# Kernel tuning notes

Hardware: AMD Instinct MI355X
Metric: run time of the kernel (lower is better)

## Reference

```python
import jax, jax.numpy as jnp
import numpy as np

NODE_DIM = 256
EDGE_DIM = 64
TIME_DIM = 1024
HEADS = 8
HEAD_DIM = NODE_DIM // HEADS
MLP = 2
BS, N = 32, 48
BN = BS * N
E = BS * N * (N - 1)


def _lin(k, fin, fout):
    return jax.random.normal(k, (fin, fout), dtype=jnp.float32) / np.sqrt(fin)


def _edge_index():
    idx = np.arange(N)
    src, dst = np.meshgrid(idx, idx, indexing='ij')
    m = src != dst
    src, dst = src[m], dst[m]              # [N*(N-1)] per graph
    offs = (np.arange(BS) * N)[:, None]
    row = (offs + src[None, :]).reshape(-1)
    col = (offs + dst[None, :]).reshape(-1)
    return jnp.asarray(np.stack([row, col]), dtype=jnp.int32)


def setup_inputs() -> dict:
    key = jax.random.key(0)
    ks = jax.random.split(key, 32)
    d = {
        'pos': jax.random.normal(ks[0], (BN, 3), jnp.float32),
        'h': jax.random.normal(ks[1], (BN, NODE_DIM), jnp.float32),
        'edge_attr': jax.random.normal(ks[2], (E, EDGE_DIM), jnp.float32),
        'node_mask': jnp.ones((BN, 1), jnp.float32),
        'node_time_emb': jax.random.normal(ks[3], (BN, TIME_DIM), jnp.float32),
        'edge_time_emb': jax.random.normal(ks[4], (E, TIME_DIM), jnp.float32),
        'edge_index': _edge_index(),
        # edge_emb: Linear(edge_dim+1 -> edge_dim)
        'W_ee': _lin(ks[5], EDGE_DIM + 1, EDGE_DIM), 'b_ee': jnp.zeros((EDGE_DIM,)),
        # AdaLN time MLPs (SiLU -> Linear)
        'W_nt': _lin(ks[6], TIME_DIM, 6 * NODE_DIM), 'b_nt': jnp.zeros((6 * NODE_DIM,)),
        'W_et': _lin(ks[7], TIME_DIM, 6 * EDGE_DIM), 'b_et': jnp.zeros((6 * EDGE_DIM,)),
        # Trans_Layer sparse attention
        'Wq': _lin(ks[8], NODE_DIM, NODE_DIM), 'bq': jnp.zeros((NODE_DIM,)),
        'Wk': _lin(ks[9], NODE_DIM, NODE_DIM), 'bk': jnp.zeros((NODE_DIM,)),
        'Wv': _lin(ks[10], NODE_DIM, NODE_DIM), 'bv': jnp.zeros((NODE_DIM,)),
        'We0': _lin(ks[11], EDGE_DIM, NODE_DIM),
        'We1': _lin(ks[12], EDGE_DIM, NODE_DIM),
        'W_n2e': _lin(ks[13], NODE_DIM, EDGE_DIM), 'b_n2e': jnp.zeros((EDGE_DIM,)),
        # node FFN
        'W_ff1': _lin(ks[14], NODE_DIM, MLP * NODE_DIM), 'b_ff1': jnp.zeros((MLP * NODE_DIM,)),
        'W_ff2': _lin(ks[15], MLP * NODE_DIM, NODE_DIM), 'b_ff2': jnp.zeros((NODE_DIM,)),
        # edge FFN
        'W_ff3': _lin(ks[16], EDGE_DIM, MLP * EDGE_DIM), 'b_ff3': jnp.zeros((MLP * EDGE_DIM,)),
        'W_ff4': _lin(ks[17], MLP * EDGE_DIM, EDGE_DIM), 'b_ff4': jnp.zeros((EDGE_DIM,)),
        # CondEquiUpdate
        'coors_scale': jnp.full((1,), 0.01, jnp.float32),
        'W_ut': _lin(ks[18], TIME_DIM, 2 * NODE_DIM), 'b_ut': jnp.zeros((2 * NODE_DIM,)),
        'W_ui': _lin(ks[19], 2 * NODE_DIM + EDGE_DIM + 1, NODE_DIM), 'b_ui': jnp.zeros((NODE_DIM,)),
        'W_uc1': _lin(ks[20], NODE_DIM, NODE_DIM), 'b_uc1': jnp.zeros((NODE_DIM,)),
        'W_uc2': _lin(ks[21], NODE_DIM, 1),
    }
    return d


def _ln(x):  # LayerNorm, no affine, eps=1e-6
    m = x.mean(-1, keepdims=True)
    v = ((x - m) ** 2).mean(-1, keepdims=True)
    return (x - m) * jax.lax.rsqrt(v + 1e-6)


def _modulate(x, shift, scale):
    return x * (1 + scale) + shift


def _block(pos, h, edge_attr, node_mask, node_time_emb, edge_time_emb, edge_index,
           W_ee, b_ee, W_nt, b_nt, W_et, b_et, Wq, bq, Wk, bk, Wv, bv, We0, We1,
           W_n2e, b_n2e, W_ff1, b_ff1, W_ff2, b_ff2, W_ff3, b_ff3, W_ff4, b_ff4,
           coors_scale, W_ut, b_ut, W_ui, b_ui, W_uc1, b_uc1, W_uc2):
    row, col = edge_index[0], edge_index[1]  # row = source j, col = target i
    diff = pos[row] - pos[col]                              # [E,3]
    dist = jnp.sqrt(jnp.sum(diff * diff, -1, keepdims=True) + 1e-12)  # [E,1]
    ea = jnp.concatenate([dist, edge_attr], -1) @ W_ee + b_ee

    nt = jax.nn.silu(node_time_emb) @ W_nt + b_nt
    n_sh_msa, n_sc_msa, n_g_msa, n_sh_mlp, n_sc_mlp, n_g_mlp = jnp.split(nt, 6, axis=1)
    et = jax.nn.silu(edge_time_emb) @ W_et + b_et
    e_sh_msa, e_sc_msa, e_g_msa, e_sh_mlp, e_sc_mlp, e_g_mlp = jnp.split(et, 6, axis=1)

    hh = _modulate(_ln(h), n_sh_msa, n_sc_msa)
    ea = _modulate(_ln(ea), e_sh_msa, e_sc_msa)

    # sparse multi-head attention over edges (Trans_Layer)
    q = (hh @ Wq + bq).reshape(BN, HEADS, HEAD_DIM)
    k = (hh @ Wk + bk).reshape(BN, HEADS, HEAD_DIM)
    v = (hh @ Wv + bv).reshape(BN, HEADS, HEAD_DIM)
    e0 = (ea @ We0).reshape(E, HEADS, HEAD_DIM)
    e1 = (ea @ We1).reshape(E, HEADS, HEAD_DIM)
    alpha = jnp.sum(q[col] * k[row] * e0, -1) / np.sqrt(HEAD_DIM)  # [E,H]
    mx = jax.ops.segment_max(alpha, col, num_segments=BN)
    ex = jnp.exp(alpha - mx[col])
    den = jax.ops.segment_sum(ex, col, num_segments=BN)
    att = ex / (den[col] + 1e-16)
    msg = v[row] * e1 * att[:, :, None]
    h_node = jax.ops.segment_sum(msg, col, num_segments=BN).reshape(BN, NODE_DIM)

    h_edge = (h_node[row] + h_node[col]) @ W_n2e + b_n2e

    h_node = h + n_g_msa * h_node
    h_node = _modulate(_ln(h_node), n_sh_mlp, n_sc_mlp) * node_mask
    ff = jax.nn.silu(h_node @ W_ff1 + b_ff1) @ W_ff2 + b_ff2
    h_out = (h_node + n_g_mlp * ff) * node_mask

    h_e = edge_attr + e_g_msa * h_edge
    h_e = _modulate(_ln(h_e), e_sh_mlp, e_sc_mlp)
    ffe = jax.nn.silu(h_e @ W_ff3 + b_ff3) @ W_ff4 + b_ff4
    h_edge_out = h_e + e_g_mlp * ffe

    # CondEquiUpdate: equivariant coordinate update
    h_input = jnp.concatenate([h_out[row], h_out[col], h_edge_out, dist], -1)
    nrm = jnp.linalg.norm(diff, axis=-1, keepdims=True)
    cdiff = diff / jnp.clip(nrm, 1e-8) * coors_scale        # CoorsNorm(scale_init=0.01)
    t_shift, t_scale = jnp.split(jax.nn.silu(edge_time_emb) @ W_ut + b_ut, 2, axis=1)
    inv = _modulate(_ln(h_input @ W_ui + b_ui), t_shift, t_scale)
    inv = jnp.tanh(jax.nn.silu(inv @ W_uc1 + b_uc1) @ W_uc2)  # [E,1]
    trans = cdiff * inv
    pos_out = pos + jax.ops.segment_sum(trans, row, num_segments=BN)
    return h_out, h_edge_out, pos_out


def reference(pos, h, edge_attr, node_mask, node_time_emb, edge_time_emb, edge_index,
              W_ee, b_ee, W_nt, b_nt, W_et, b_et, Wq, bq, Wk, bk, Wv, bv, We0, We1,
              W_n2e, b_n2e, W_ff1, b_ff1, W_ff2, b_ff2, W_ff3, b_ff3, W_ff4, b_ff4,
              coors_scale, W_ut, b_ut, W_ui, b_ui, W_uc1, b_uc1, W_uc2):
    return _block(pos, h, edge_attr, node_mask, node_time_emb, edge_time_emb, edge_index,
                  W_ee, b_ee, W_nt, b_nt, W_et, b_et, Wq, bq, Wk, bk, Wv, bv, We0, We1,
                  W_n2e, b_n2e, W_ff1, b_ff1, W_ff2, b_ff2, W_ff3, b_ff3, W_ff4, b_ff4,
                  coors_scale, W_ut, b_ut, W_ui, b_ui, W_uc1, b_uc1, W_uc2)
```

## Files before the change

### kernel.cpp

```cpp
#include <hip/hip_runtime.h>

typedef unsigned short u16;
typedef __attribute__((ext_vector_type(4))) u16 u16x4;
typedef __attribute__((ext_vector_type(8))) u16 u16x8;
typedef __attribute__((ext_vector_type(8))) short s16x8;
typedef __attribute__((ext_vector_type(4))) float f32x4;

#define E_CNT 72192
#define BN_CNT 1536
#define EPG 2256

__device__ __forceinline__ float b2f(u16 u) {
    union { unsigned int i; float f; } x; x.i = ((unsigned int)u) << 16; return x.f;
}
__device__ __forceinline__ u16 f2b(float f) {
    union { float f; unsigned int i; } x; x.f = f;
    unsigned int r = x.i + 0x7fffu + ((x.i >> 16) & 1u);
    return (u16)(r >> 16);
}
__device__ __forceinline__ float siluf(float x) { return x / (1.f + expf(-x)); }

__device__ __forceinline__ void gll16(const void* g, void* l) {
    __builtin_amdgcn_global_load_lds(
        (const __attribute__((address_space(1))) void*)g,
        (__attribute__((address_space(3))) void*)l, 16, 0, 0);
}

__device__ __forceinline__ float wave_ln64(float x) {
    float s = x;
    #pragma unroll
    for (int off = 1; off < 64; off <<= 1) s += __shfl_xor(s, off);
    float mean = s * 0.015625f;
    float d = x - mean;
    float v2 = d * d;
    #pragma unroll
    for (int off = 1; off < 64; off <<= 1) v2 += __shfl_xor(v2, off);
    return d * rsqrtf(v2 * 0.015625f + 1e-6f);
}

__device__ __forceinline__ float block_ln256(float x) {
    __shared__ float tmp[4];
    int t = threadIdx.x;
    float s = x;
    #pragma unroll
    for (int off = 1; off < 64; off <<= 1) s += __shfl_xor(s, off);
    if ((t & 63) == 0) tmp[t >> 6] = s;
    __syncthreads();
    float mean = (tmp[0] + tmp[1] + tmp[2] + tmp[3]) * (1.f / 256.f);
    float d = x - mean;
    float v2 = d * d;
    #pragma unroll
    for (int off = 1; off < 64; off <<= 1) v2 += __shfl_xor(v2, off);
    __syncthreads();
    if ((t & 63) == 0) tmp[t >> 6] = v2;
    __syncthreads();
    float var = (tmp[0] + tmp[1] + tmp[2] + tmp[3]) * (1.f / 256.f);
    return d * rsqrtf(var + 1e-6f);
}

template<int ACT, int OUTBF>
__global__ __launch_bounds__(256) void k_gemm(
    const u16* __restrict__ A, const u16* __restrict__ Bt,
    const float* __restrict__ bias, void* __restrict__ C,
    int M, int N, int K)
{
    __shared__ u16 As[64][40];
    __shared__ u16 Bs[64][40];
    int bn0 = blockIdx.x * 64, bm0 = blockIdx.y * 64;
    int t = threadIdx.x;
    int lane = t & 63, wave = t >> 6;
    int wm = wave >> 1, wn = wave & 1;
    int lr = t >> 2, lc = (t & 3) * 8;
    f32x4 acc[2][2] = {};
    const u16* Ap = A + (size_t)(bm0 + lr) * K + lc;
    const u16* Bp = Bt + (size_t)(bn0 + lr) * K + lc;
    int fr = lane & 15, fk = (lane >> 4) * 8;
    for (int k0 = 0; k0 < K; k0 += 32) {
        *(u16x8*)&As[lr][lc] = *(const u16x8*)(Ap + k0);
        *(u16x8*)&Bs[lr][lc] = *(const u16x8*)(Bp + k0);
        __syncthreads();
        s16x8 a0 = *(const s16x8*)&As[wm * 32 + fr][fk];
        s16x8 a1 = *(const s16x8*)&As[wm * 32 + 16 + fr][fk];
        s16x8 b0 = *(const s16x8*)&Bs[wn * 32 + fr][fk];
        s16x8 b1 = *(const s16x8*)&Bs[wn * 32 + 16 + fr][fk];
        acc[0][0] = __builtin_amdgcn_mfma_f32_16x16x32_bf16(a0, b0, acc[0][0], 0, 0, 0);
        acc[0][1] = __builtin_amdgcn_mfma_f32_16x16x32_bf16(a0, b1, acc[0][1], 0, 0, 0);
        acc[1][0] = __builtin_amdgcn_mfma_f32_16x16x32_bf16(a1, b0, acc[1][0], 0, 0, 0);
        acc[1][1] = __builtin_amdgcn_mfma_f32_16x16x32_bf16(a1, b1, acc[1][1], 0, 0, 0);
        __syncthreads();
    }
    int cIn = lane & 15, r4 = (lane >> 4) * 4;
    #pragma unroll
    for (int i = 0; i < 2; i++)
    #pragma unroll
    for (int j = 0; j < 2; j++) {
        int col = bn0 + wn * 32 + j * 16 + cIn;
        float bv = bias ? bias[col] : 0.f;
        #pragma unroll
        for (int r = 0; r < 4; r++) {
            int rowg = bm0 + wm * 32 + i * 16 + r4 + r;
            float vv = acc[i][j][r] + bv;
            if (ACT == 1) vv = siluf(vv);
            if (OUTBF) ((u16*)C)[(size_t)rowg * N + col] = f2b(vv);
            else       ((float*)C)[(size_t)rowg * N + col] = vv;
        }
    }
}

template<int ACT, int OUTBF>
__global__ __launch_bounds__(256) void k_gemm128(
    const u16* __restrict__ A, const u16* __restrict__ Bt,
    const float* __restrict__ bias, void* __restrict__ C,
    int M, int N, int K)
{
    __shared__ u16 As[3][128 * 32];
    __shared__ u16 Bs[3][128 * 32];
    const int t = threadIdx.x;
    const int lane = t & 63, wv = t >> 6;
    const int wm = wv >> 1, wn = wv & 1;
    const int nwg = gridDim.x * gridDim.y;
    const int orig = blockIdx.y * gridDim.x + blockIdx.x;
    const int q8 = nwg >> 3, r8 = nwg & 7;
    const int xcd = orig & 7, lin = orig >> 3;
    const int wgid = (xcd < r8 ? xcd * (q8 + 1) : r8 * (q8 + 1) + (xcd - r8) * q8) + lin;
    const int bxs = wgid % gridDim.x, bys = wgid / gridDim.x;
    const int bn0 = bxs * 128, bm0 = bys * 128;
    const int srow = t >> 2;
    const int scol = ((t & 3) ^ ((t >> 3) & 3)) * 8;
    const u16* Ap = A + (size_t)(bm0 + srow) * K + scol;
    const u16* Bp = Bt + (size_t)(bn0 + srow) * K + scol;
    const size_t rstep = (size_t)64 * K;
    const int woff = wv * 16 * 32;
    const int fr = lane & 15;
    const int fkc = (((lane >> 4) ^ ((fr >> 1) & 3)) * 8);
    f32x4 acc[4][4] = {};
    const int NT = K >> 5;

    auto STAGE = [&](int b, int ko) {
        gll16(Ap + ko, &As[b][woff]);
        gll16(Ap + ko + rstep, &As[b][woff + 64 * 32]);
        gll16(Bp + ko, &Bs[b][woff]);
        gll16(Bp + ko + rstep, &Bs[b][woff + 64 * 32]);
    };
    auto COMPUTE = [&](int b) {
        const u16* aBase = &As[b][wm * 64 * 32];
        const u16* bBase = &Bs[b][wn * 64 * 32];
        s16x8 af[4], bfr[4];
        #pragma unroll
        for (int m = 0; m < 4; m++) af[m] = *(const s16x8*)&aBase[(m * 16 + fr) * 32 + fkc];
        #pragma unroll
        for (int n = 0; n < 4; n++) bfr[n] = *(const s16x8*)&bBase[(n * 16 + fr) * 32 + fkc];
        #pragma unroll
        for (int m = 0; m < 4; m++)
        #pragma unroll
        for (int n = 0; n < 4; n++)
            acc[m][n] = __builtin_amdgcn_mfma_f32_16x16x32_bf16(af[m], bfr[n], acc[m][n], 0, 0, 0);
    };

    STAGE(0, 0);
    if (NT > 1) STAGE(1, 32);
    int cur = 0;
    for (int tt = 0; tt < NT; tt++) {
        if (tt + 2 < NT) STAGE((cur + 2) % 3, (tt + 2) * 32);
        __builtin_amdgcn_sched_barrier(0);
        int ahead = NT - 1 - tt; if (ahead > 2) ahead = 2;
        if (ahead == 2)      asm volatile("s_waitcnt vmcnt(8)" ::: "memory");
        else if (ahead == 1) asm volatile("s_waitcnt vmcnt(4)" ::: "memory");
        else                 asm volatile("s_waitcnt vmcnt(0)" ::: "memory");
        __builtin_amdgcn_sched_barrier(0);
        __builtin_amdgcn_s_barrier();
        COMPUTE(cur);
        __builtin_amdgcn_s_barrier();
        __builtin_amdgcn_sched_barrier(0);
        cur = (cur + 1) % 3;
    }

    const int cIn = lane & 15, r4 = (lane >> 4) * 4;
    #pragma unroll
    for (int n = 0; n < 4; n++) {
        int col = bn0 + wn * 64 + n * 16 + cIn;
        float bv = bias ? bias[col] : 0.f;
        #pragma unroll
        for (int m = 0; m < 4; m++) {
            #pragma unroll
            for (int r = 0; r < 4; r++) {
                int rowg = bm0 + wm * 64 + m * 16 + r4 + r;
                float vv = acc[m][n][r] + bv;
                if (ACT == 1) vv = siluf(vv);
                if (OUTBF) ((u16*)C)[(size_t)rowg * N + col] = f2b(vv);
                else       ((float*)C)[(size_t)rowg * N + col] = vv;
            }
        }
    }
}

struct ConvJob { const float* W; u16* Wt; int ldw, k0, n0, K, tile_start, tiles_k; };
struct CopyJob { const float* src; float* dst; int n; };
struct BatchArgs { ConvJob cj[17]; CopyJob cp[5]; int conv_blocks; };

__global__ __launch_bounds__(256) void k_prep(BatchArgs a)
{
    __shared__ float ls[64][65];
    int b = blockIdx.x;
    int t = threadIdx.x;
    if (b < a.conv_blocks) {
        int j = 0;
        #pragma unroll 1
        while (j + 1 < 17 && a.cj[j + 1].tile_start <= b) ++j;
        const ConvJob J = a.cj[j];
        int local = b - J.tile_start;
        int tk = local % J.tiles_k, tn = local / J.tiles_k;
        int k0 = tk * 64, n0 = tn * 64;
        int cn = t & 63, rk = t >> 6;
        #pragma unroll
        for (int p = 0; p < 16; p++) {
            int kk = p * 4 + rk;
            ls[kk][cn] = J.W[(size_t)(J.k0 + k0 + kk) * J.ldw + J.n0 + n0 + cn];
        }
        __syncthreads();
        int ck = t & 63, rn = t >> 6;
        #pragma unroll
        for (int p = 0; p < 16; p++) {
            int nn = p * 4 + rn;
            J.Wt[(size_t)(n0 + nn) * J.K + k0 + ck] = f2b(ls[ck][nn]);
        }
    } else {
        int c = b - a.conv_blocks;
        const CopyJob C = a.cp[c];
        for (int i = t; i < C.n; i += 256) C.dst[i] = C.src[i];
    }
}

__global__ void k_silu_bf(const float* __restrict__ in, u16* __restrict__ out, int n4)
{
    int i = blockIdx.x * 256 + threadIdx.x;
    int stride = gridDim.x * 256;
    for (; i < n4; i += stride) {
        f32x4 v = *(const f32x4*)(in + (size_t)i * 4);
        u16x4 o;
        #pragma unroll
        for (int j = 0; j < 4; j++) o[j] = f2b(siluf(v[j]));
        *(u16x4*)(out + (size_t)i * 4) = o;
    }
}

__global__ __launch_bounds__(256) void k_edge_pre(
    const float* __restrict__ pos, const float* __restrict__ edge_attr,
    const int* __restrict__ ei, const float* __restrict__ W_ee,
    const float* __restrict__ b_ee, const float* __restrict__ coors_scale,
    const u16* __restrict__ etf,
    u16* __restrict__ ea_mod, float* __restrict__ dist, float* __restrict__ cdiff)
{
    __shared__ float Ws[65][64];
    int t = threadIdx.x;
    for (int i = t; i < 65 * 64; i += 256) Ws[i >> 6][i & 63] = W_ee[i];
    __syncthreads();
    int l = t & 63;
    float bee = b_ee[l];
    float cscale = coors_scale[0];
    for (int g = 0; g < 16; g++) {
        int e = blockIdx.x * 64 + g * 4 + (t >> 6);
        int row = ei[e], col = ei[E_CNT + e];
        float d0 = pos[row * 3 + 0] - pos[col * 3 + 0];
        float d1 = pos[row * 3 + 1] - pos[col * 3 + 1];
        float d2 = pos[row * 3 + 2] - pos[col * 3 + 2];
        float ssq = d0 * d0 + d1 * d1 + d2 * d2;
        float dst = sqrtf(ssq + 1e-12f);
        float nrm = sqrtf(ssq);
        float cs = cscale / fmaxf(nrm, 1e-8f);
        if (l == 0) {
            dist[e] = dst;
            cdiff[e * 3 + 0] = d0 * cs; cdiff[e * 3 + 1] = d1 * cs; cdiff[e * 3 + 2] = d2 * cs;
        }
        float attr = edge_attr[(size_t)e * 64 + l];
        float acc = dst * Ws[0][l];
        for (int f = 0; f < 64; f++) acc += __shfl(attr, f) * Ws[1 + f][l];
        acc += bee;
        float y = wave_ln64(acc);
        const u16* ep = etf + (size_t)e * 896;
        float m = y * (1.f + b2f(ep[64 + l])) + b2f(ep[l]);
        ea_mod[(size_t)e * 64 + l] = f2b(m);
    }
}

__global__ __launch_bounds__(256) void k_node_hh(
    const float* __restrict__ h, const float* __restrict__ nt, u16* __restrict__ hh)
{
    int n = blockIdx.x, c = threadIdx.x;
    float x = h[(size_t)n * 256 + c];
    float y = block_ln256(x);
    float m = y * (1.f + nt[(size_t)n * 1536 + 256 + c]) + nt[(size_t)n * 1536 + c];
    hh[(size_t)n * 256 + c] = f2b(m);
}

__global__ __launch_bounds__(256) void k_agg(
    const float* __restrict__ qkv, const u16* __restrict__ e01,
    float* __restrict__ hnode, u16* __restrict__ hnode_bf)
{
    int n = blockIdx.x;
    int b = n / 48, i = n % 48;
    int t = threadIdx.x;
    __shared__ float qs[8][33];
    __shared__ float att[47][8];
    __shared__ float mxs[8], dens[8];
    __shared__ int elist[47], slist[47];
    qs[t >> 5][t & 31] = qkv[(size_t)n * 768 + t];
    if (t < 47) {
        int s = t + (t >= i ? 1 : 0);
        slist[t] = s;
        elist[t] = b * EPG + s * 47 + (i < s ? i : i - 1);
    }
    __syncthreads();
    for (int idx = t; idx < 376; idx += 256) {
        int j = idx >> 3, hh = idx & 7;
        int src = b * 48 + slist[j];
        int e = elist[j];
        const float* kp = qkv + (size_t)src * 768 + 256 + hh * 32;
        const u16* ep = e01 + (size_t)e * 512 + hh * 32;
        float p = 0.f;
        #pragma unroll
        for (int d = 0; d < 32; d++) p += qs[hh][d] * kp[d] * b2f(ep[d]);
        att[j][hh] = p * 0.17677669529663687f;
    }
    __syncthreads();
    if (t < 8) {
        float m = -1e30f;
        for (int j = 0; j < 47; j++) m = fmaxf(m, att[j][t]);
        float den = 0.f;
        for (int j = 0; j < 47; j++) den += expf(att[j][t] - m);
        mxs[t] = m; dens[t] = den + 1e-16f;
    }
    __syncthreads();
    for (int idx = t; idx < 376; idx += 256) {
        int j = idx >> 3, hh = idx & 7;
        att[j][hh] = expf(att[j][hh] - mxs[hh]) / dens[hh];
    }
    __syncthreads();
    int c = t, hh = t >> 5;
    float acc = 0.f;
    for (int j = 0; j < 47; j++) {
        int src = b * 48 + slist[j];
        int e = elist[j];
        acc += att[j][hh] * qkv[(size_t)src * 768 + 512 + c] * b2f(e01[(size_t)e * 512 + 256 + c]);
    }
    hnode[(size_t)n * 256 + c] = acc;
    hnode_bf[(size_t)n * 256 + c] = f2b(acc);
}

__global__ __launch_bounds__(256) void k_node_mod(
    const float* __restrict__ h, const float* __restrict__ hnode_raw,
    const float* __restrict__ nt, const float* __restrict__ mask,
    float* __restrict__ hmod, u16* __restrict__ hmod_bf)
{
    int n = blockIdx.x, c = threadIdx.x;
    float x = h[(size_t)n * 256 + c] + nt[(size_t)n * 1536 + 512 + c] * hnode_raw[(size_t)n * 256 + c];
    float y = block_ln256(x);
    float m = (y * (1.f + nt[(size_t)n * 1536 + 1024 + c]) + nt[(size_t)n * 1536 + 768 + c]) * mask[n];
    hmod[(size_t)n * 256 + c] = m;
    hmod_bf[(size_t)n * 256 + c] = f2b(m);
}

__global__ void k_hout(const float* __restrict__ hmod, const float* __restrict__ ff2,
                       const float* __restrict__ nt, const float* __restrict__ mask,
                       float* __restrict__ out, u16* __restrict__ hout_bf)
{
    int i = blockIdx.x * 256 + threadIdx.x;
    if (i >= BN_CNT * 256) return;
    int n = i >> 8, c = i & 255;
    float v = (hmod[i] + nt[(size_t)n * 1536 + 1280 + c] * ff2[i]) * mask[n];
    out[i] = v;
    hout_bf[i] = f2b(v);
}

__global__ __launch_bounds__(256) void k_edge_mod(
    const float* __restrict__ Q1, const float* __restrict__ b_n2e,
    const float* __restrict__ edge_attr, const int* __restrict__ ei,
    const u16* __restrict__ etf, float* __restrict__ hemod, u16* __restrict__ hemod_bf)
{
    int e = blockIdx.x * 4 + (threadIdx.x >> 6);
    int l = threadIdx.x & 63;
    int row = ei[e], col = ei[E_CNT + e];
    float hedge = Q1[(size_t)row * 64 + l] + Q1[(size_t)col * 64 + l] + b_n2e[l];
    const u16* ep = etf + (size_t)e * 896;
    float x = edge_attr[(size_t)e * 64 + l] + b2f(ep[128 + l]) * hedge;
    float y = wave_ln64(x);
    float m = y * (1.f + b2f(ep[256 + l])) + b2f(ep[192 + l]);
    hemod[(size_t)e * 64 + l] = m;
    hemod_bf[(size_t)e * 64 + l] = f2b(m);
}

__global__ void k_edge_out(const float* __restrict__ hemod, const float* __restrict__ ff4,
                           const u16* __restrict__ etf,
                           float* __restrict__ out2, u16* __restrict__ heout_bf)
{
    size_t i = (size_t)blockIdx.x * 256 + threadIdx.x;
    if (i >= (size_t)E_CNT * 64) return;
    int e = (int)(i >> 6), c = (int)(i & 63);
    float v = hemod[i] + b2f(etf[(size_t)e * 896 + 320 + c]) * ff4[i];
    out2[i] = v;
    heout_bf[i] = f2b(v);
}

__global__ __launch_bounds__(256) void k_inv_pre(
    const float* __restrict__ p12,
    const u16* __restrict__ P3, const float* __restrict__ dist,
    const float* __restrict__ W_ui, const float* __restrict__ b_ui,
    const int* __restrict__ ei, const u16* __restrict__ etf, u16* __restrict__ invmod)
{
    int e = blockIdx.x, c = threadIdx.x;
    int row = ei[e], col = ei[E_CNT + e];
    float x = p12[(size_t)row * 512 + c] + p12[(size_t)col * 512 + 256 + c]
            + b2f(P3[(size_t)e * 256 + c]) + dist[e] * W_ui[576 * 256 + c] + b_ui[c];
    float y = block_ln256(x);
    const u16* ep = etf + (size_t)e * 896;
    float m = y * (1.f + b2f(ep[640 + c])) + b2f(ep[384 + c]);
    invmod[(size_t)e * 256 + c] = f2b(m);
}

__global__ __launch_bounds__(256) void k_inv(const u16* __restrict__ uc1,
                                             const float* __restrict__ W_uc2,
                                             float* __restrict__ inv)
{
    int e = blockIdx.x * 4 + (threadIdx.x >> 6);
    int l = threadIdx.x & 63;
    u16x4 v = *(const u16x4*)(uc1 + (size_t)e * 256 + l * 4);
    const float* w = W_uc2 + l * 4;
    float s = b2f(v[0]) * w[0] + b2f(v[1]) * w[1] + b2f(v[2]) * w[2] + b2f(v[3]) * w[3];
    #pragma unroll
    for (int off = 1; off < 64; off <<= 1) s += __shfl_xor(s, off);
    if (l == 0) inv[e] = tanhf(s);
}

__global__ void k_pos(const float* __restrict__ pos, const float* __restrict__ cdiff,
                      const float* __restrict__ inv, float* __restrict__ out3)
{
    int n = blockIdx.x * 256 + threadIdx.x;
    if (n >= BN_CNT) return;
    int b = n / 48, s = n % 48;
    int e0 = b * EPG + s * 47;
    float a0 = 0.f, a1 = 0.f, a2 = 0.f;
    for (int j = 0; j < 47; j++) {
        float f = inv[e0 + j];
        a0 += cdiff[(size_t)(e0 + j) * 3 + 0] * f;
        a1 += cdiff[(size_t)(e0 + j) * 3 + 1] * f;
        a2 += cdiff[(size_t)(e0 + j) * 3 + 2] * f;
    }
    out3[n * 3 + 0] = pos[n * 3 + 0] + a0;
    out3[n * 3 + 1] = pos[n * 3 + 1] + a1;
    out3[n * 3 + 2] = pos[n * 3 + 2] + a2;
}

extern "C" void kernel_launch(void* const* d_in, const int* in_sizes, int n_in,
                              void* d_out, int out_size, void* d_ws, size_t ws_size,
                              hipStream_t stream)
{
    (void)in_sizes; (void)n_in; (void)out_size; (void)ws_size;
    const float* pos       = (const float*)d_in[0];
    const float* h         = (const float*)d_in[1];
    const float* edge_attr = (const float*)d_in[2];
    const float* node_mask = (const float*)d_in[3];
    const float* nte       = (const float*)d_in[4];
    const float* ete       = (const float*)d_in[5];
    const int*   ei        = (const int*)d_in[6];
    const float* W_ee = (const float*)d_in[7];  const float* b_ee = (const float*)d_in[8];
    const float* W_nt = (const float*)d_in[9];  const float* b_nt = (const float*)d_in[10];
    const float* W_et = (const float*)d_in[11]; const float* b_et = (const float*)d_in[12];
    const float* Wq  = (const float*)d_in[13];  const float* bq  = (const float*)d_in[14];
    const float* Wk  = (const float*)d_in[15];  const float* bk  = (const float*)d_in[16];
    const float* Wv  = (const float*)d_in[17];  const float* bv  = (const float*)d_in[18];
    const float* We0 = (const float*)d_in[19];  const float* We1 = (const float*)d_in[20];
    const float* W_n2e = (const float*)d_in[21]; const float* b_n2e = (const float*)d_in[22];
    const float* W_ff1 = (const float*)d_in[23]; const float* b_ff1 = (const float*)d_in[24];
    const float* W_ff2 = (const float*)d_in[25]; const float* b_ff2 = (const float*)d_in[26];
    const float* W_ff3 = (const float*)d_in[27]; const float* b_ff3 = (const float*)d_in[28];
    const float* W_ff4 = (const float*)d_in[29]; const float* b_ff4 = (const float*)d_in[30];
    const float* coors_scale = (const float*)d_in[31];
    const float* W_ut = (const float*)d_in[32]; const float* b_ut = (const float*)d_in[33];
    const float* W_ui = (const float*)d_in[34]; const float* b_ui = (const float*)d_in[35];
    const float* W_uc1 = (const float*)d_in[36]; const float* b_uc1 = (const float*)d_in[37];
    const float* W_uc2 = (const float*)d_in[38];

    const size_t E = E_CNT;
    char* ws = (char*)d_ws;
    size_t off = 0;
    auto AL = [&](size_t b) { size_t o = off; off += (b + 255) & ~(size_t)255; return o; };

    size_t o_wtcat  = AL(896 * 1024 * 2);
    size_t o_wtnt   = AL(1536 * 1024 * 2);
    size_t o_wtqkv  = AL(768 * 256 * 2);
    size_t o_wte01  = AL(512 * 64 * 2);
    size_t o_wtn2e  = AL(64 * 256 * 2);
    size_t o_wtff1  = AL(512 * 256 * 2), o_wtff2 = AL(256 * 512 * 2);
    size_t o_wtff3  = AL(128 * 64 * 2),  o_wtff4 = AL(64 * 128 * 2);
    size_t o_wtuiab = AL(512 * 256 * 2);
    size_t o_wtuic  = AL(256 * 64 * 2),  o_wtuc1 = AL(256 * 256 * 2);
    size_t o_bias896 = AL(896 * 4);
    size_t o_bias768 = AL(768 * 4);
    size_t o_reg1 = AL(E * 1024 * 2);
    size_t o_etf  = AL(E * 896 * 2);
    size_t o_ntes = AL(1536 * 1024 * 2);
    size_t o_ntf  = AL((size_t)1536 * 1536 * 4);
    size_t o_eamod = AL(E * 64 * 2);
    size_t o_dist = AL(E * 4), o_cdiff = AL(E * 12);
    size_t o_qkv  = AL(1536 * 768 * 4);
    size_t o_reg3 = AL(E * 512 * 2);
    size_t o_hnode = AL(1536 * 256 * 4), o_hnodebf = AL(1536 * 256 * 2);
    size_t o_q1 = AL(1536 * 64 * 4);
    size_t o_hh = AL(1536 * 256 * 2);
    size_t o_hmod = AL(1536 * 256 * 4), o_hmodbf = AL(1536 * 256 * 2);
    size_t o_ff1 = AL(1536 * 512 * 2), o_ff2 = AL(1536 * 256 * 4);
    size_t o_houtbf = AL(1536 * 256 * 2);
    size_t o_hemod = AL(E * 64 * 4), o_hemodbf = AL(E * 64 * 2);
    size_t o_p12 = AL(1536 * 512 * 4);
    size_t o_inv = AL(E * 4);
    size_t o_etes = o_reg1;
    size_t o_p3 = o_reg1;
    size_t o_invmod = o_reg1 + E * 256 * 2;
    size_t o_uc1o = o_reg1 + E * 256 * 4;
    size_t o_e01 = o_reg3;
    size_t o_ffem = o_reg3;
    size_t o_ff4o = o_reg3 + E * 128 * 2;
    size_t o_heoutbf = o_reg3 + E * 128 * 2 + E * 64 * 4;

    #define WSU(o) ((u16*)(ws + (o)))
    #define WSF(o) ((float*)(ws + (o)))

    {
        BatchArgs a;
        int s = 0; int j = 0;
        auto add = [&](const float* W, u16* Wt, int ldw, int k0, int n0, int K, int NC) {
            a.cj[j++] = ConvJob{W, Wt, ldw, k0, n0, K, s, K / 64};
            s += (K / 64) * (NC / 64);
        };
        add(W_et, WSU(o_wtcat), 384, 0, 0, 1024, 384);
        add(W_ut, WSU(o_wtcat) + (size_t)384 * 1024, 512, 0, 0, 1024, 512);
        add(W_nt, WSU(o_wtnt), 1536, 0, 0, 1024, 1536);
        add(Wq, WSU(o_wtqkv), 256, 0, 0, 256, 256);
        add(Wk, WSU(o_wtqkv) + (size_t)256 * 256, 256, 0, 0, 256, 256);
        add(Wv, WSU(o_wtqkv) + (size_t)512 * 256, 256, 0, 0, 256, 256);
        add(We0, WSU(o_wte01), 256, 0, 0, 64, 256);
        add(We1, WSU(o_wte01) + (size_t)256 * 64, 256, 0, 0, 64, 256);
        add(W_n2e, WSU(o_wtn2e), 64, 0, 0, 256, 64);
        add(W_ff1, WSU(o_wtff1), 512, 0, 0, 256, 512);
        add(W_ff2, WSU(o_wtff2), 256, 0, 0, 512, 256);
        add(W_ff3, WSU(o_wtff3), 128, 0, 0, 64, 128);
        add(W_ff4, WSU(o_wtff4), 64, 0, 0, 128, 64);
        add(W_ui, WSU(o_wtuiab), 256, 0, 0, 256, 256);
        add(W_ui, WSU(o_wtuiab) + (size_t)256 * 256, 256, 256, 0, 256, 256);
        add(W_ui, WSU(o_wtuic), 256, 512, 0, 64, 256);
        add(W_uc1, WSU(o_wtuc1), 256, 0, 0, 256, 256);
        a.conv_blocks = s;
        a.cp[0] = CopyJob{b_et, WSF(o_bias896), 384};
        a.cp[1] = CopyJob{b_ut, WSF(o_bias896) + 384, 512};
        a.cp[2] = CopyJob{bq, WSF(o_bias768), 256};
        a.cp[3] = CopyJob{bk, WSF(o_bias768) + 256, 256};
        a.cp[4] = CopyJob{bv, WSF(o_bias768) + 512, 256};
        k_prep<<<s + 5, 256, 0, stream>>>(a);
    }

    k_silu_bf<<<2048, 256, 0, stream>>>(ete, WSU(o_etes), (int)(E * 1024 / 4));
    k_silu_bf<<<1024, 256, 0, stream>>>(nte, WSU(o_ntes), 1536 * 1024 / 4);

    k_gemm128<0, 1><<<dim3(7, 564), 256, 0, stream>>>(WSU(o_etes), WSU(o_wtcat), WSF(o_bias896), WSU(o_etf), E_CNT, 896, 1024);
    k_gemm<0, 0><<<dim3(24, 24), 256, 0, stream>>>(WSU(o_ntes), WSU(o_wtnt), b_nt, WSF(o_ntf), 1536, 1536, 1024);

    k_edge_pre<<<1128, 256, 0, stream>>>(pos, edge_attr, ei, W_ee, b_ee, coors_scale,
                                         WSU(o_etf), WSU(o_eamod), WSF(o_dist), WSF(o_cdiff));

    k_node_hh<<<1536, 256, 0, stream>>>(h, WSF(o_ntf), WSU(o_hh));
    k_gemm<0, 0><<<dim3(12, 24), 256, 0, stream>>>(WSU(o_hh), WSU(o_wtqkv), WSF(o_bias768), WSF(o_qkv), 1536, 768, 256);
    k_gemm128<0, 1><<<dim3(4, 564), 256, 0, stream>>>(WSU(o_eamod), WSU(o_wte01), nullptr, WSU(o_e01), E_CNT, 512, 64);
    k_agg<<<1536, 256, 0, stream>>>(WSF(o_qkv), WSU(o_e01), WSF(o_hnode), WSU(o_hnodebf));

    k_gemm<0, 0><<<dim3(1, 24), 256, 0, stream>>>(WSU(o_hnodebf), WSU(o_wtn2e), nullptr, WSF(o_q1), 1536, 64, 256);

    k_node_mod<<<1536, 256, 0, stream>>>(h, WSF(o_hnode), WSF(o_ntf), node_mask, WSF(o_hmod), WSU(o_hmodbf));
    k_gemm<1, 1><<<dim3(8, 24), 256, 0, stream>>>(WSU(o_hmodbf), WSU(o_wtff1), b_ff1, WSU(o_ff1), 1536, 512, 256);
    k_gemm<0, 0><<<dim3(4, 24), 256, 0, stream>>>(WSU(o_ff1), WSU(o_wtff2), b_ff2, WSF(o_ff2), 1536, 256, 512);
    k_hout<<<1536, 256, 0, stream>>>(WSF(o_hmod), WSF(o_ff2), WSF(o_ntf), node_mask, (float*)d_out, WSU(o_houtbf));

    k_edge_mod<<<18048, 256, 0, stream>>>(WSF(o_q1), b_n2e, edge_attr, ei, WSU(o_etf), WSF(o_hemod), WSU(o_hemodbf));
    k_gemm128<1, 1><<<dim3(1, 564), 256, 0, stream>>>(WSU(o_hemodbf), WSU(o_wtff3), b_ff3, WSU(o_ffem), E_CNT, 128, 64);
    k_gemm<0, 0><<<dim3(1, 1128), 256, 0, stream>>>(WSU(o_ffem), WSU(o_wtff4), b_ff4, WSF(o_ff4o), E_CNT, 64, 128);
    k_edge_out<<<18048, 256, 0, stream>>>(WSF(o_hemod), WSF(o_ff4o), WSU(o_etf),
                                          (float*)d_out + 393216, WSU(o_heoutbf));

    k_gemm<0, 0><<<dim3(8, 24), 256, 0, stream>>>(WSU(o_houtbf), WSU(o_wtuiab), nullptr, WSF(o_p12), 1536, 512, 256);
    k_gemm128<0, 1><<<dim3(2, 564), 256, 0, stream>>>(WSU(o_heoutbf), WSU(o_wtuic), nullptr, WSU(o_p3), E_CNT, 256, 64);
    k_inv_pre<<<E_CNT, 256, 0, stream>>>(WSF(o_p12), WSU(o_p3), WSF(o_dist),
                                         W_ui, b_ui, ei, WSU(o_etf), WSU(o_invmod));
    k_gemm128<1, 1><<<dim3(2, 564), 256, 0, stream>>>(WSU(o_invmod), WSU(o_wtuc1), b_uc1, WSU(o_uc1o), E_CNT, 256, 256);
    k_inv<<<18048, 256, 0, stream>>>(WSU(o_uc1o), W_uc2, WSF(o_inv));
    k_pos<<<6, 256, 0, stream>>>(pos, WSF(o_cdiff), WSF(o_inv), (float*)d_out + 393216 + E_CNT * 64);

    #undef WSU
    #undef WSF
}
```

Measured before the change: 742.2 us.

## Fuse SiLU and bf16 conversion into the edge time-embedding GEMM A-load

Adds a 128x128 GEMM variant that loads fp32 edge time embeddings straight into registers, applies SiLU and rounds to bf16 while writing them into LDS. This removes the separate SiLU pass and its large bf16 intermediate buffer. Only the B operand still uses async global-to-LDS loads. The trade-off is that A is now read as fp32 (twice the bytes) once per N-tile, and SiLU is recomputed in every column block. Separately, the node time GEMM moves from the small-tile kernel to the 128-tile kernel, which uses fewer, larger workgroups.

```diff
diff --git a/kernel.cpp b/kernel.cpp
--- a/kernel.cpp
+++ b/kernel.cpp
@@ -187,6 +187,128 @@
                 int rowg = bm0 + wm * 64 + m * 16 + r4 + r;
                 float vv = acc[m][n][r] + bv;
                 if (ACT == 1) vv = siluf(vv);
+                if (OUTBF) ((u16*)C)[(size_t)rowg * N + col] = f2b(vv);
+                else       ((float*)C)[(size_t)rowg * N + col] = vv;
+            }
+        }
+    }
+}
+
+struct AReg { f32x4 a, b, c, d; };
+
+template<int OUTBF>
+__global__ __launch_bounds__(256) void k_gemm128_fs(
+    const float* __restrict__ A32, const u16* __restrict__ Bt,
+    const float* __restrict__ bias, void* __restrict__ C,
+    int M, int N, int K)
+{
+    __shared__ u16 As[3][128 * 32];
+    __shared__ u16 Bs[3][128 * 32];
+    const int t = threadIdx.x;
+    const int lane = t & 63, wv = t >> 6;
+    const int wm = wv >> 1, wn = wv & 1;
+    const int nwg = gridDim.x * gridDim.y;
+    const int orig = blockIdx.y * gridDim.x + blockIdx.x;
+    const int q8 = nwg >> 3, r8 = nwg & 7;
+    const int xcd = orig & 7, lin = orig >> 3;
+    const int wgid = (xcd < r8 ? xcd * (q8 + 1) : r8 * (q8 + 1) + (xcd - r8) * q8) + lin;
+    const int bxs = wgid % gridDim.x, bys = wgid / gridDim.x;
+    const int bn0 = bxs * 128, bm0 = bys * 128;
+    const int srow = t >> 2;
+    const int scol = ((t & 3) ^ ((t >> 3) & 3)) * 8;
+    const float* Ap = A32 + (size_t)(bm0 + srow) * K + scol;
+    const u16* Bp = Bt + (size_t)(bn0 + srow) * K + scol;
+    const size_t rstep = (size_t)64 * K;
+    const int woff = wv * 16 * 32;
+    const int dA = wv * 512 + lane * 8;
+    const int fr = lane & 15;
+    const int fkc = (((lane >> 4) ^ ((fr >> 1) & 3)) * 8);
+    f32x4 acc[4][4] = {};
+    const int NT = K >> 5;
+    const int koMax = K - 32;
+
+    auto LOADA = [&](AReg& r, int ko) {
+        int k = ko > koMax ? koMax : ko;
+        r.a = *(const f32x4*)(Ap + k);
+        r.b = *(const f32x4*)(Ap + k + 4);
+        r.c = *(const f32x4*)(Ap + k + rstep);
+        r.d = *(const f32x4*)(Ap + k + rstep + 4);
+    };
+    auto WRITEA = [&](int b, const AReg& r) {
+        u16x8 w0, w1;
+        #pragma unroll
+        for (int j = 0; j < 4; j++) {
+            w0[j] = f2b(siluf(r.a[j]));  w0[4 + j] = f2b(siluf(r.b[j]));
+            w1[j] = f2b(siluf(r.c[j]));  w1[4 + j] = f2b(siluf(r.d[j]));
+        }
+        *(u16x8*)&As[b][dA] = w0;
+        *(u16x8*)&As[b][2048 + dA] = w1;
+    };
+    auto STAGEB = [&](int b, int ko) {
+        int k = ko > koMax ? koMax : ko;
+        gll16(Bp + k, &Bs[b][woff]);
+        gll16(Bp + k + rstep, &Bs[b][woff + 2048]);
+    };
+    auto COMPUTE = [&](int b) {
+        const u16* aBase = &As[b][wm * 64 * 32];
+        const u16* bBase = &Bs[b][wn * 64 * 32];
+        s16x8 af[4], bfr[4];
+        #pragma unroll
+        for (int m = 0; m < 4; m++) af[m] = *(const s16x8*)&aBase[(m * 16 + fr) * 32 + fkc];
+        #pragma unroll
+        for (int n = 0; n < 4; n++) bfr[n] = *(const s16x8*)&bBase[(n * 16 + fr) * 32 + fkc];
+        #pragma unroll
+        for (int m = 0; m < 4; m++)
+        #pragma unroll
+        for (int n = 0; n < 4; n++)
+            acc[m][n] = __builtin_amdgcn_mfma_f32_16x16x32_bf16(af[m], bfr[n], acc[m][n], 0, 0, 0);
+    };
+
+    AReg rE, rO;
+    LOADA(rE, 0);  STAGEB(0, 0);
+    LOADA(rO, 32); STAGEB(1, 32);
+    int cur = 0;
+    #pragma unroll 1
+    for (int tt = 0; tt < NT; tt += 2) {
+        WRITEA(cur, rE);
+        __builtin_amdgcn_sched_barrier(0);
+        LOADA(rE, (tt + 2) * 32);
+        STAGEB((cur + 2) % 3, (tt + 2) * 32);
+        __builtin_amdgcn_sched_barrier(0);
+        asm volatile("s_waitcnt vmcnt(12)" ::: "memory");
+        asm volatile("s_waitcnt lgkmcnt(0)" ::: "memory");
+        __builtin_amdgcn_sched_barrier(0);
+        __builtin_amdgcn_s_barrier();
+        COMPUTE(cur);
+        __builtin_amdgcn_s_barrier();
+        __builtin_amdgcn_sched_barrier(0);
+        cur = (cur + 1) % 3;
+        WRITEA(cur, rO);
+        __builtin_amdgcn_sched_barrier(0);
+        LOADA(rO, (tt + 3) * 32);
+        STAGEB((cur + 2) % 3, (tt + 3) * 32);
+        __builtin_amdgcn_sched_barrier(0);
+        asm volatile("s_waitcnt vmcnt(12)" ::: "memory");
+        asm volatile("s_waitcnt lgkmcnt(0)" ::: "memory");
+        __builtin_amdgcn_sched_barrier(0);
+        __builtin_amdgcn_s_barrier();
+        COMPUTE(cur);
+        __builtin_amdgcn_s_barrier();
+        __builtin_amdgcn_sched_barrier(0);
+        cur = (cur + 1) % 3;
+    }
+
+    const int cIn = lane & 15, r4 = (lane >> 4) * 4;
+    #pragma unroll
+    for (int n = 0; n < 4; n++) {
+        int col = bn0 + wn * 64 + n * 16 + cIn;
+        float bv = bias ? bias[col] : 0.f;
+        #pragma unroll
+        for (int m = 0; m < 4; m++) {
+            #pragma unroll
+            for (int r = 0; r < 4; r++) {
+                int rowg = bm0 + wm * 64 + m * 16 + r4 + r;
+                float vv = acc[m][n][r] + bv;
                 if (OUTBF) ((u16*)C)[(size_t)rowg * N + col] = f2b(vv);
                 else       ((float*)C)[(size_t)rowg * N + col] = vv;
             }
@@ -513,7 +635,6 @@
     size_t o_hemod = AL(E * 64 * 4), o_hemodbf = AL(E * 64 * 2);
     size_t o_p12 = AL(1536 * 512 * 4);
     size_t o_inv = AL(E * 4);
-    size_t o_etes = o_reg1;
     size_t o_p3 = o_reg1;
     size_t o_invmod = o_reg1 + E * 256 * 2;
     size_t o_uc1o = o_reg1 + E * 256 * 4;
@@ -558,11 +679,12 @@
         k_prep<<<s + 5, 256, 0, stream>>>(a);
     }
 
-    k_silu_bf<<<2048, 256, 0, stream>>>(ete, WSU(o_etes), (int)(E * 1024 / 4));
     k_silu_bf<<<1024, 256, 0, stream>>>(nte, WSU(o_ntes), 1536 * 1024 / 4);
 
-    k_gemm128<0, 1><<<dim3(7, 564), 256, 0, stream>>>(WSU(o_etes), WSU(o_wtcat), WSF(o_bias896), WSU(o_etf), E_CNT, 896, 1024);
-    k_gemm<0, 0><<<dim3(24, 24), 256, 0, stream>>>(WSU(o_ntes), WSU(o_wtnt), b_nt, WSF(o_ntf), 1536, 1536, 1024);
+    k_gemm128_fs<1><<<dim3(7, 564), 256, 0, stream>>>(
+        ete, WSU(o_wtcat), WSF(o_bias896), WSU(o_etf), E_CNT, 896, 1024);
+    k_gemm128<0, 0><<<dim3(12, 12), 256, 0, stream>>>(
+        WSU(o_ntes), WSU(o_wtnt), b_nt, WSF(o_ntf), 1536, 1536, 1024);
 
     k_edge_pre<<<1128, 256, 0, stream>>>(pos, edge_attr, ei, W_ee, b_ee, coors_scale,
                                          WSU(o_etf), WSU(o_eamod), WSF(o_dist), WSF(o_cdiff));
```

Result: slower. 953.4 us (+28.5%).
